# Optimization experiments

Hardware: AMD Instinct MI355X
Metric: run time of the kernel (lower is better)

The kernel has to match this reference:

```python
import jax, jax.numpy as jnp
import numpy as np
import math

DIM = 1280
NUM_HEADS = 16
HEAD_DIM = DIM // NUM_HEADS  # 80
MLP_HIDDEN = 4 * DIM         # 5120
N = 4096
EPS = 1e-6


def setup_inputs() -> dict:
    key = jax.random.key(0)
    ks = jax.random.split(key, 12)
    s = 0.02
    inp = {
        "hidden_states": jax.random.normal(ks[0], (N, DIM), jnp.float32),
        "rotary_pos_emb": jax.random.normal(ks[1], (N, HEAD_DIM // 2), jnp.float32),
        "cu_seqlens": jnp.array([0, 1024, 2048, 3072, 4096], jnp.int32),
        "norm1_w": jnp.ones((DIM,), jnp.float32),
        "norm1_b": jnp.zeros((DIM,), jnp.float32),
        "norm2_w": jnp.ones((DIM,), jnp.float32),
        "norm2_b": jnp.zeros((DIM,), jnp.float32),
        "qkv_w": jax.random.normal(ks[2], (3 * DIM, DIM), jnp.float32) * s,
        "qkv_b": jnp.zeros((3 * DIM,), jnp.float32),
        "proj_w": jax.random.normal(ks[3], (DIM, DIM), jnp.float32) * s,
        "proj_b": jnp.zeros((DIM,), jnp.float32),
        "fc1_w": jax.random.normal(ks[4], (MLP_HIDDEN, DIM), jnp.float32) * s,
        "fc1_b": jnp.zeros((MLP_HIDDEN,), jnp.float32),
        "fc2_w": jax.random.normal(ks[5], (DIM, MLP_HIDDEN), jnp.float32) * s,
        "fc2_b": jnp.zeros((DIM,), jnp.float32),
    }
    return inp


def _layernorm(x, w, b):
    m = jnp.mean(x, axis=-1, keepdims=True)
    v = jnp.mean(jnp.square(x - m), axis=-1, keepdims=True)
    return (x - m) * jax.lax.rsqrt(v + EPS) * w + b


def _apply_rope(t, cos, sin):
    # t: [N, H, hd]; cos/sin: [N, 1, hd]
    x1 = t[..., : HEAD_DIM // 2]
    x2 = t[..., HEAD_DIM // 2:]
    rot = jnp.concatenate([-x2, x1], axis=-1)
    return t * cos + rot * sin


def _quick_gelu(x):
    return x * jax.nn.sigmoid(1.702 * x)


def reference(hidden_states, rotary_pos_emb, cu_seqlens,
              norm1_w, norm1_b, norm2_w, norm2_b,
              qkv_w, qkv_b, proj_w, proj_b,
              fc1_w, fc1_b, fc2_w, fc2_b):
    n = hidden_states.shape[0]
    # ---- attention branch (pre-norm) ----
    x = _layernorm(hidden_states, norm1_w, norm1_b)
    qkv = (x @ qkv_w.T + qkv_b).reshape(n, 3, NUM_HEADS, HEAD_DIM)
    q, k, v = qkv[:, 0], qkv[:, 1], qkv[:, 2]  # [N, H, hd]
    # rotary: freqs [N, hd//2] -> tiled cos/sin [N, 1, hd]
    cos = jnp.cos(rotary_pos_emb)
    sin = jnp.sin(rotary_pos_emb)
    cos = jnp.concatenate([cos, cos], axis=-1)[:, None, :]
    sin = jnp.concatenate([sin, sin], axis=-1)[:, None, :]
    q = _apply_rope(q, cos, sin)
    k = _apply_rope(k, cos, sin)
    # block-diagonal varlen mask from cu_seqlens via segment ids
    seg = jnp.searchsorted(cu_seqlens[1:], jnp.arange(n, dtype=cu_seqlens.dtype), side="right")
    allowed = seg[:, None] == seg[None, :]  # [N, N] bool
    scores = jnp.einsum("qhd,khd->hqk", q, k) / math.sqrt(HEAD_DIM)
    scores = jnp.where(allowed[None], scores, jnp.finfo(scores.dtype).min)
    attn = jax.nn.softmax(scores.astype(jnp.float32), axis=-1).astype(q.dtype)
    out = jnp.einsum("hqk,khd->qhd", attn, v).reshape(n, DIM)
    out = out @ proj_w.T + proj_b
    h = hidden_states + out
    # ---- MLP branch (pre-norm) ----
    y = _layernorm(h, norm2_w, norm2_b)
    y = _quick_gelu(y @ fc1_w.T + fc1_b) @ fc2_w.T + fc2_b
    return h + y
```

## Files before the change

kernel.cpp:

```cpp
#include <hip/hip_runtime.h>
#include <hip/hip_bf16.h>


typedef __bf16 bf16_t;
typedef bf16_t bf16x8 __attribute__((ext_vector_type(8)));
typedef bf16_t bf16x4 __attribute__((ext_vector_type(4)));
typedef float f32x4 __attribute__((ext_vector_type(4)));

#define DIM 1280
#define NHEADS 16
#define HDIM 80
#define MLP 5120
#define NTOK 4096
#define QKV_N 3840

#define GLOAD_LDS16(gp, lp)                                                          \
    __builtin_amdgcn_global_load_lds((const __attribute__((address_space(1))) void*)(gp), \
                                     (__attribute__((address_space(3))) void*)(lp), 16, 0, 0)

__global__ void cvt_f32_bf16(const float* __restrict__ in, bf16_t* __restrict__ out, int n) {
    int i = (blockIdx.x * blockDim.x + threadIdx.x) * 4;
    int stride = gridDim.x * blockDim.x * 4;
    for (; i < n; i += stride) {
        float4 v = *(const float4*)(in + i);
        bf16x4 o;
        o[0] = (bf16_t)v.x; o[1] = (bf16_t)v.y; o[2] = (bf16_t)v.z; o[3] = (bf16_t)v.w;
        *(bf16x4*)(out + i) = o;
    }
}

__global__ void seg_kernel(const int* __restrict__ cu, int ncu, int* __restrict__ seg, int n) {
    int i = blockIdx.x * blockDim.x + threadIdx.x;
    if (i >= n) return;
    int s = 0;
    for (int j = 1; j < ncu - 1; j++) if (i >= cu[j]) s = j;
    seg[i] = s;
}

__global__ __launch_bounds__(256) void ln_kernel(const float* __restrict__ x,
                                                 const float* __restrict__ w,
                                                 const float* __restrict__ b,
                                                 bf16_t* __restrict__ out) {
    int row = blockIdx.x;
    const float* xr = x + (long)row * DIM;
    float v[5];
    float s = 0.f, ss = 0.f;
#pragma unroll
    for (int j = 0; j < 5; j++) {
        v[j] = xr[j * 256 + threadIdx.x];
        s += v[j];
        ss += v[j] * v[j];
    }
#pragma unroll
    for (int off = 32; off > 0; off >>= 1) {
        s += __shfl_xor(s, off, 64);
        ss += __shfl_xor(ss, off, 64);
    }
    __shared__ float red[8];
    int wid = threadIdx.x >> 6;
    if ((threadIdx.x & 63) == 0) { red[wid] = s; red[wid + 4] = ss; }
    __syncthreads();
    s = red[0] + red[1] + red[2] + red[3];
    ss = red[4] + red[5] + red[6] + red[7];
    float mean = s * (1.f / DIM);
    float var = ss * (1.f / DIM) - mean * mean;
    float rstd = rsqrtf(var + 1e-6f);
    bf16_t* orow = out + (long)row * DIM;
#pragma unroll
    for (int j = 0; j < 5; j++) {
        int d = j * 256 + threadIdx.x;
        orow[d] = (bf16_t)((v[j] - mean) * rstd * w[d] + b[d]);
    }
}

__global__ __launch_bounds__(256) void prep_kernel(const bf16_t* __restrict__ qkv,
                                                   const float* __restrict__ rot,
                                                   bf16_t* __restrict__ Qd,
                                                   bf16_t* __restrict__ Kd,
                                                   bf16_t* __restrict__ Vt) {
    __shared__ bf16_t tv[64 * 88];
    const int tid = threadIdx.x;
    const int t0 = blockIdx.x * 64;
    const int h = blockIdx.y;

    for (int c = tid; c < 64 * 10; c += 256) {
        int tl = c / 10, a = c % 10;
        bf16x8 v = *(const bf16x8*)(qkv + (long)(t0 + tl) * QKV_N + 2 * DIM + h * HDIM + a * 8);
        *(bf16x8*)(tv + tl * 88 + a * 8) = v;
    }

    for (int c = tid; c < 64 * 10; c += 256) {
        int tl = c / 10, a = c % 10;
        long gq = (long)(t0 + tl) * QKV_N + h * HDIM + a * 4;
        bf16x4 q1 = *(const bf16x4*)(qkv + gq);
        bf16x4 q2 = *(const bf16x4*)(qkv + gq + 40);
        bf16x4 k1 = *(const bf16x4*)(qkv + gq + DIM);
        bf16x4 k2 = *(const bf16x4*)(qkv + gq + DIM + 40);
        float4 rv = *(const float4*)(rot + (long)(t0 + tl) * 40 + a * 4);
        float rr[4] = {rv.x, rv.y, rv.z, rv.w};
        bf16x4 oq1, oq2, ok1, ok2;
#pragma unroll
        for (int j = 0; j < 4; j++) {
            float c_, s_;
            __sincosf(rr[j], &s_, &c_);
            float x1 = (float)q1[j], x2 = (float)q2[j];
            oq1[j] = (bf16_t)(x1 * c_ - x2 * s_);
            oq2[j] = (bf16_t)(x2 * c_ + x1 * s_);
            x1 = (float)k1[j]; x2 = (float)k2[j];
            ok1[j] = (bf16_t)(x1 * c_ - x2 * s_);
            ok2[j] = (bf16_t)(x2 * c_ + x1 * s_);
        }
        long o = ((long)h * NTOK + t0 + tl) * 96 + a * 4;
        *(bf16x4*)(Qd + o) = oq1;
        *(bf16x4*)(Qd + o + 40) = oq2;
        *(bf16x4*)(Kd + o) = ok1;
        *(bf16x4*)(Kd + o + 40) = ok2;
    }
    {
        bf16x8 z;
#pragma unroll
        for (int j = 0; j < 8; j++) z[j] = (bf16_t)0.f;
        for (int c = tid; c < 64 * 2; c += 256) {
            int tl = c / 2, a = c % 2;
            long o = ((long)h * NTOK + t0 + tl) * 96 + 80 + a * 8;
            *(bf16x8*)(Qd + o) = z;
            *(bf16x8*)(Kd + o) = z;
        }
    }
    __syncthreads();

    for (int c = tid; c < 80 * 8; c += 256) {
        int d = c / 8, tc = c % 8;
        bf16x8 v;
#pragma unroll
        for (int j = 0; j < 8; j++) v[j] = tv[(tc * 8 + j) * 88 + d];
        *(bf16x8*)(Vt + ((long)h * HDIM + d) * NTOK + t0 + tc * 8) = v;
    }
}

__global__ void fc2_reduce(const float* __restrict__ p, const float* __restrict__ b,
                           float* __restrict__ out) {
    long i = (long)blockIdx.x * blockDim.x + threadIdx.x;
    float4 o = ((const float4*)out)[i];
    float4 a0 = ((const float4*)p)[i];
    float4 a1 = ((const float4*)p)[i + (long)NTOK * DIM / 4];
    int c4 = (int)(i % (DIM / 4)) * 4;
    float4 bv = *(const float4*)(b + c4);
    o.x += a0.x + a1.x + bv.x;
    o.y += a0.y + a1.y + bv.y;
    o.z += a0.z + a1.z + bv.z;
    o.w += a0.w + a1.w + bv.w;
    ((float4*)out)[i] = o;
}

template <int EPI, int NF>
__global__ __launch_bounds__(512, 2) void gemm256(const bf16_t* __restrict__ A,
                                                  const bf16_t* __restrict__ B,
                                                  const float* __restrict__ bias,
                                                  const float* __restrict__ res,
                                                  void* __restrict__ Cv,
                                                  int M, int N, int K, int kspl) {
    constexpr int SLOTB = 32768 + NF * 8192;
    __shared__ char lds[2 * SLOTB];
    const int tid = threadIdx.x;
    const int lane = tid & 63;
    const int l15 = lane & 15;
    const int g = lane >> 4;
    const int wid = tid >> 6;
    const int wr = wid >> 2;
    const int wc = wid & 3;

    const int nx = gridDim.x;
    const int id = blockIdx.y * nx + blockIdx.x;
    const int cpx = (nx * gridDim.y) >> 3;
    const int sid = (id & 7) * cpx + (id >> 3);
    const int m0 = (sid / nx) * 256;
    const int n0 = (sid % nx) * (NF * 64);
    const int k0 = blockIdx.z * kspl;
    const int NT = kspl >> 6;

    const bf16_t* gA[4]; int lAo[4];
#pragma unroll
    for (int j = 0; j < 4; j++) {
        int off = j * 8192 + tid * 16;
        int row = off >> 7;
        int cb = (off & 127) ^ ((row & 7) << 4);
        gA[j] = A + (long)(m0 + row) * K + k0 + (cb >> 1);
        lAo[j] = j * 8192 + wid * 1024;
    }
    const bf16_t* gB[NF]; int lBo[NF];
#pragma unroll
    for (int j = 0; j < NF; j++) {
        int off = j * 8192 + tid * 16;
        int row = off >> 7;
        int cb = (off & 127) ^ ((row & 7) << 4);
        gB[j] = B + (long)(n0 + row) * K + k0 + (cb >> 1);
        lBo[j] = 32768 + j * 8192 + wid * 1024;
    }

    f32x4 acc[8][NF];
#pragma unroll
    for (int i = 0; i < 8; i++)
#pragma unroll
        for (int j = 0; j < NF; j++) acc[i][j] = (f32x4){0.f, 0.f, 0.f, 0.f};

    auto stage = [&](int slot, int t) {
        char* sb = lds + slot * SLOTB;
#pragma unroll
        for (int j = 0; j < 4; j++) GLOAD_LDS16(gA[j] + t * 64, sb + lAo[j]);
#pragma unroll
        for (int j = 0; j < NF; j++) GLOAD_LDS16(gB[j] + t * 64, sb + lBo[j]);
    };

    auto tile_body = [&](int slot) {
        const char* pA = lds + slot * SLOTB;
        const char* pB = pA + 32768;
#pragma unroll
        for (int ks = 0; ks < 2; ks++) {
            bf16x8 af[8], bb[NF];
#pragma unroll
            for (int n = 0; n < NF; n++) {
                int r = wc * (NF * 16) + n * 16 + l15;
                bb[n] = *(const bf16x8*)(pB + r * 128 + ((ks * 64 + g * 16) ^ ((r & 7) << 4)));
            }
#pragma unroll
            for (int m = 0; m < 8; m++) {
                int r = wr * 128 + m * 16 + l15;
                af[m] = *(const bf16x8*)(pA + r * 128 + ((ks * 64 + g * 16) ^ ((r & 7) << 4)));
            }
            asm volatile("s_waitcnt lgkmcnt(0)" ::: "memory");
            __builtin_amdgcn_sched_barrier(0);
            __builtin_amdgcn_s_setprio(1);
#pragma unroll
            for (int m = 0; m < 8; m++)
#pragma unroll
                for (int n = 0; n < NF; n++)
                    acc[m][n] = __builtin_amdgcn_mfma_f32_16x16x32_bf16(af[m], bb[n],
                                                                        acc[m][n], 0, 0, 0);
            __builtin_amdgcn_s_setprio(0);
        }
    };

    stage(0, 0);
    stage(1, 1);

    for (int t = 0; t < NT; ++t) {
        if (t < NT - 1) {
            if constexpr (NF == 4)
                asm volatile("s_waitcnt vmcnt(8)\n\ts_barrier" ::: "memory");
            else
                asm volatile("s_waitcnt vmcnt(9)\n\ts_barrier" ::: "memory");
        } else {
            asm volatile("s_waitcnt vmcnt(0)\n\ts_barrier" ::: "memory");
        }
        tile_body(t & 1);
        if (t + 2 < NT) {
            asm volatile("s_barrier" ::: "memory");
            stage(t & 1, t + 2);
        }
    }

#pragma unroll
    for (int m = 0; m < 8; m++)
#pragma unroll
        for (int n = 0; n < NF; n++) {
            const int col = n0 + wc * (NF * 16) + n * 16 + l15;
            const float bv = (EPI == 3) ? 0.f : bias[col];
#pragma unroll
            for (int rr = 0; rr < 4; rr++) {
                const int row = m0 + wr * 128 + m * 16 + g * 4 + rr;
                const long idx = (long)row * N + col;
                float val = acc[m][n][rr] + bv;
                if (EPI == 0) {
                    ((bf16_t*)Cv)[idx] = (bf16_t)val;
                } else if (EPI == 1) {
                    ((float*)Cv)[idx] = res[idx] + val;
                } else if (EPI == 2) {
                    float ge = val / (1.f + __expf(-1.702f * val));
                    ((bf16_t*)Cv)[idx] = (bf16_t)ge;
                } else {
                    ((float*)Cv)[(long)blockIdx.z * M * N + idx] = val;
                }
            }
        }
}

__global__ __launch_bounds__(256) void attn_kernel(const bf16_t* __restrict__ Qd,
                                                   const bf16_t* __restrict__ Kd,
                                                   const bf16_t* __restrict__ Vt,
                                                   const int* __restrict__ seg,
                                                   const int* __restrict__ cu,
                                                   bf16_t* __restrict__ out) {
    __shared__ bf16_t lK[64 * 104];
    __shared__ bf16_t lV[80 * 72];
    __shared__ bf16_t lP[4 * 16 * 72];

    const int tid = threadIdx.x;
    const int lane = tid & 63;
    const int l15 = lane & 15;
    const int g = lane >> 4;
    const int wid = tid >> 6;
    const int h = blockIdx.y;
    const int q0 = blockIdx.x * 64;

    bf16x8 aq[3];
    {
        const bf16_t* qp = Qd + ((long)h * NTOK + q0 + wid * 16 + l15) * 96;
#pragma unroll
        for (int ks = 0; ks < 3; ks++)
            aq[ks] = *(const bf16x8*)(qp + ks * 32 + g * 8);
    }
    int segq[4];
#pragma unroll
    for (int r = 0; r < 4; r++) segq[r] = seg[q0 + wid * 16 + g * 4 + r];
    const int kbeg = cu[seg[q0]];
    const int kend = cu[seg[q0 + 63] + 1];

    const float scale = 0.111803398874989485f;
    float mI[4], lI[4];
    f32x4 o[5];
#pragma unroll
    for (int r = 0; r < 4; r++) { mI[r] = -1e30f; lI[r] = 0.f; }
#pragma unroll
    for (int n = 0; n < 5; n++) o[n] = (f32x4){0.f, 0.f, 0.f, 0.f};

    for (int kt = kbeg; kt < kend; kt += 64) {
        for (int c = tid; c < 64 * 12; c += 256) {
            int row = c / 12, c16 = c % 12;
            bf16x8 v = *(const bf16x8*)(Kd + ((long)h * NTOK + kt + row) * 96 + c16 * 8);
            *(bf16x8*)(lK + row * 104 + c16 * 8) = v;
        }
        for (int c = tid; c < 80 * 8; c += 256) {
            int d = c / 8, a = c % 8;
            bf16x8 v = *(const bf16x8*)(Vt + ((long)h * HDIM + d) * NTOK + kt + a * 8);
            *(bf16x8*)(lV + d * 72 + a * 8) = v;
        }
        __syncthreads();

        f32x4 s[4];
#pragma unroll
        for (int n = 0; n < 4; n++) s[n] = (f32x4){0.f, 0.f, 0.f, 0.f};
#pragma unroll
        for (int n = 0; n < 4; n++)
#pragma unroll
            for (int ks = 0; ks < 3; ks++) {
                bf16x8 kf = *(const bf16x8*)(lK + (n * 16 + l15) * 104 + ks * 32 + g * 8);
                s[n] = __builtin_amdgcn_mfma_f32_16x16x32_bf16(aq[ks], kf, s[n], 0, 0, 0);
            }

        float sv[4][4];
#pragma unroll
        for (int n = 0; n < 4; n++) {
            int kg = kt + n * 16 + l15;
            int sk = seg[kg];
#pragma unroll
            for (int r = 0; r < 4; r++)
                sv[n][r] = (sk == segq[r]) ? s[n][r] * scale : -3.0e38f;
        }

        float nm[4], al[4], ps[4];
#pragma unroll
        for (int r = 0; r < 4; r++) {
            float x = fmaxf(fmaxf(sv[0][r], sv[1][r]), fmaxf(sv[2][r], sv[3][r]));
#pragma unroll
            for (int off = 8; off >= 1; off >>= 1) x = fmaxf(x, __shfl_xor(x, off, 64));
            nm[r] = fmaxf(mI[r], x);
            al[r] = __expf(mI[r] - nm[r]);
            ps[r] = 0.f;
        }
#pragma unroll
        for (int n = 0; n < 4; n++)
#pragma unroll
            for (int r = 0; r < 4; r++) {
                float p = __expf(sv[n][r] - nm[r]);
                ps[r] += p;
                lP[wid * 1152 + (g * 4 + r) * 72 + n * 16 + l15] = (bf16_t)p;
            }
#pragma unroll
        for (int r = 0; r < 4; r++) {
            float x = ps[r];
#pragma unroll
            for (int off = 8; off >= 1; off >>= 1) x += __shfl_xor(x, off, 64);
            lI[r] = lI[r] * al[r] + x;
            mI[r] = nm[r];
        }
#pragma unroll
        for (int n = 0; n < 5; n++)
#pragma unroll
            for (int r = 0; r < 4; r++) o[n][r] *= al[r];

        asm volatile("s_waitcnt lgkmcnt(0)" ::: "memory");
        bf16x8 pa[2];
#pragma unroll
        for (int ks = 0; ks < 2; ks++)
            pa[ks] = *(const bf16x8*)(lP + wid * 1152 + l15 * 72 + ks * 32 + g * 8);
#pragma unroll
        for (int n = 0; n < 5; n++)
#pragma unroll
            for (int ks = 0; ks < 2; ks++) {
                bf16x8 vb = *(const bf16x8*)(lV + (n * 16 + l15) * 72 + ks * 32 + g * 8);
                o[n] = __builtin_amdgcn_mfma_f32_16x16x32_bf16(pa[ks], vb, o[n], 0, 0, 0);
            }
        __syncthreads();
    }

#pragma unroll
    for (int n = 0; n < 5; n++)
#pragma unroll
        for (int r = 0; r < 4; r++) {
            int row = q0 + wid * 16 + g * 4 + r;
            out[(long)row * DIM + h * HDIM + n * 16 + l15] = (bf16_t)(o[n][r] / lI[r]);
        }
}

extern "C" void kernel_launch(void* const* d_in, const int* in_sizes, int n_in,
                              void* d_out, int out_size, void* d_ws, size_t ws_size,
                              hipStream_t stream) {
    const float* hidden = (const float*)d_in[0];
    const float* rot    = (const float*)d_in[1];
    const int*   cu     = (const int*)d_in[2];
    const float* n1w    = (const float*)d_in[3];
    const float* n1b    = (const float*)d_in[4];
    const float* n2w    = (const float*)d_in[5];
    const float* n2b    = (const float*)d_in[6];
    const float* qkv_w  = (const float*)d_in[7];
    const float* qkv_b  = (const float*)d_in[8];
    const float* proj_w = (const float*)d_in[9];
    const float* proj_b = (const float*)d_in[10];
    const float* fc1_w  = (const float*)d_in[11];
    const float* fc1_b  = (const float*)d_in[12];
    const float* fc2_w  = (const float*)d_in[13];
    const float* fc2_b  = (const float*)d_in[14];
    float* outp = (float*)d_out;

    char* ws = (char*)d_ws;
    bf16_t* w2   = (bf16_t*)(ws);
    bf16_t* w1   = (bf16_t*)(ws + 13107200);
    bf16_t* wp   = (bf16_t*)(ws + 26214400);
    bf16_t* wq   = (bf16_t*)(ws + 29491200);
    bf16_t* xln  = (bf16_t*)(ws + 39321600);
    bf16_t* qkvb = (bf16_t*)(ws + 49807360);
    bf16_t* Qd   = (bf16_t*)(ws + 81264640);
    bf16_t* Kd   = (bf16_t*)(ws + 93847552);
    bf16_t* Vt   = (bf16_t*)(ws + 106430464);
    bf16_t* attno= (bf16_t*)(ws + 116916224);
    bf16_t* act  = (bf16_t*)(ws + 49807360);
    float*  p01  = (float*)(ws + 91750400);
    int*    seg  = (int*)(ws + 133693440);

    int ncu = in_sizes[2];

    cvt_f32_bf16<<<2048, 256, 0, stream>>>(qkv_w, wq, QKV_N * DIM);
    cvt_f32_bf16<<<1024, 256, 0, stream>>>(proj_w, wp, DIM * DIM);
    cvt_f32_bf16<<<2048, 256, 0, stream>>>(fc1_w, w1, MLP * DIM);
    cvt_f32_bf16<<<2048, 256, 0, stream>>>(fc2_w, w2, DIM * MLP);
    seg_kernel<<<(NTOK + 255) / 256, 256, 0, stream>>>(cu, ncu, seg, NTOK);

    ln_kernel<<<NTOK, 256, 0, stream>>>(hidden, n1w, n1b, xln);
    gemm256<0, 5><<<dim3(QKV_N / 320, NTOK / 256, 1), 512, 0, stream>>>(
        xln, wq, qkv_b, nullptr, qkvb, NTOK, QKV_N, DIM, DIM);
    prep_kernel<<<dim3(NTOK / 64, NHEADS), 256, 0, stream>>>(qkvb, rot, Qd, Kd, Vt);
    attn_kernel<<<dim3(NTOK / 64, NHEADS), 256, 0, stream>>>(Qd, Kd, Vt, seg, cu, attno);
    gemm256<1, 4><<<dim3(DIM / 256, NTOK / 256, 1), 512, 0, stream>>>(
        attno, wp, proj_b, hidden, outp, NTOK, DIM, DIM, DIM);
    ln_kernel<<<NTOK, 256, 0, stream>>>(outp, n2w, n2b, xln);
    gemm256<2, 5><<<dim3(MLP / 320, NTOK / 256, 1), 512, 0, stream>>>(
        xln, w1, fc1_b, nullptr, act, NTOK, MLP, DIM, DIM);
    gemm256<3, 4><<<dim3(DIM / 256, NTOK / 256, 2), 512, 0, stream>>>(
        act, w2, nullptr, nullptr, p01, NTOK, DIM, MLP, 2560);
    fc2_reduce<<<NTOK * DIM / 4 / 256, 256, 0, stream>>>(p01, fc2_b, outp);
}
```

Measured before the change: 378.8 us.

## Rewrite GEMM with 4-stage BK=32 LDS pipeline and split-K proj

Replaces the double-buffered BK=64 GEMM, which had variable N-tile width, with a fixed 256x256-tile kernel. The new kernel uses BK=32 slices in four LDS buffers, prefetching three tiles ahead and issuing the next stage before the MMA work to overlap loads with compute. The proj GEMM becomes a split-K=2 GEMM writing fp32 partials, followed by a reduce kernel that adds bias and the residual, so the small 80-block grid gets more parallelism. The cost is extra partial-sum memory traffic and an additional launch, plus a different QKV/FC1 tile shape with more blocks.

```diff
diff --git a/kernel.cpp b/kernel.cpp
--- a/kernel.cpp
+++ b/kernel.cpp
@@ -138,30 +138,27 @@
     }
 }
 
-__global__ void fc2_reduce(const float* __restrict__ p, const float* __restrict__ b,
-                           float* __restrict__ out) {
+__global__ void reduce2(const float* __restrict__ p, const float* __restrict__ b,
+                        const float* __restrict__ res, float* __restrict__ out) {
     long i = (long)blockIdx.x * blockDim.x + threadIdx.x;
-    float4 o = ((const float4*)out)[i];
+    float4 r = ((const float4*)res)[i];
     float4 a0 = ((const float4*)p)[i];
     float4 a1 = ((const float4*)p)[i + (long)NTOK * DIM / 4];
     int c4 = (int)(i % (DIM / 4)) * 4;
     float4 bv = *(const float4*)(b + c4);
-    o.x += a0.x + a1.x + bv.x;
-    o.y += a0.y + a1.y + bv.y;
-    o.z += a0.z + a1.z + bv.z;
-    o.w += a0.w + a1.w + bv.w;
+    float4 o = {r.x + a0.x + a1.x + bv.x, r.y + a0.y + a1.y + bv.y,
+                r.z + a0.z + a1.z + bv.z, r.w + a0.w + a1.w + bv.w};
     ((float4*)out)[i] = o;
 }
 
-template <int EPI, int NF>
-__global__ __launch_bounds__(512, 2) void gemm256(const bf16_t* __restrict__ A,
-                                                  const bf16_t* __restrict__ B,
-                                                  const float* __restrict__ bias,
-                                                  const float* __restrict__ res,
-                                                  void* __restrict__ Cv,
-                                                  int M, int N, int K, int kspl) {
-    constexpr int SLOTB = 32768 + NF * 8192;
-    __shared__ char lds[2 * SLOTB];
+template <int EPI>
+__global__ __launch_bounds__(512, 2) void gemmP(const bf16_t* __restrict__ A,
+                                                const bf16_t* __restrict__ B,
+                                                const float* __restrict__ bias,
+                                                const float* __restrict__ res,
+                                                void* __restrict__ Cv,
+                                                int M, int N, int K, int kspl) {
+    __shared__ char lds[4 * 32768];
     const int tid = threadIdx.x;
     const int lane = tid & 63;
     const int l15 = lane & 15;
@@ -175,96 +172,77 @@
     const int cpx = (nx * gridDim.y) >> 3;
     const int sid = (id & 7) * cpx + (id >> 3);
     const int m0 = (sid / nx) * 256;
-    const int n0 = (sid % nx) * (NF * 64);
+    const int n0 = (sid % nx) * 256;
     const int k0 = blockIdx.z * kspl;
-    const int NT = kspl >> 6;
-
-    const bf16_t* gA[4]; int lAo[4];
-#pragma unroll
-    for (int j = 0; j < 4; j++) {
+    const int NT = kspl >> 5;
+
+    const bf16_t* gA[2]; const bf16_t* gB[2]; int lAo[2], lBo[2];
+#pragma unroll
+    for (int j = 0; j < 2; j++) {
         int off = j * 8192 + tid * 16;
-        int row = off >> 7;
-        int cb = (off & 127) ^ ((row & 7) << 4);
+        int row = off >> 6;
+        int cb = (off & 63) ^ ((row & 3) << 4);
         gA[j] = A + (long)(m0 + row) * K + k0 + (cb >> 1);
+        gB[j] = B + (long)(n0 + row) * K + k0 + (cb >> 1);
         lAo[j] = j * 8192 + wid * 1024;
-    }
-    const bf16_t* gB[NF]; int lBo[NF];
-#pragma unroll
-    for (int j = 0; j < NF; j++) {
-        int off = j * 8192 + tid * 16;
-        int row = off >> 7;
-        int cb = (off & 127) ^ ((row & 7) << 4);
-        gB[j] = B + (long)(n0 + row) * K + k0 + (cb >> 1);
-        lBo[j] = 32768 + j * 8192 + wid * 1024;
-    }
-
-    f32x4 acc[8][NF];
+        lBo[j] = 16384 + j * 8192 + wid * 1024;
+    }
+
+    f32x4 acc[8][4];
 #pragma unroll
     for (int i = 0; i < 8; i++)
 #pragma unroll
-        for (int j = 0; j < NF; j++) acc[i][j] = (f32x4){0.f, 0.f, 0.f, 0.f};
-
-    auto stage = [&](int slot, int t) {
-        char* sb = lds + slot * SLOTB;
-#pragma unroll
-        for (int j = 0; j < 4; j++) GLOAD_LDS16(gA[j] + t * 64, sb + lAo[j]);
-#pragma unroll
-        for (int j = 0; j < NF; j++) GLOAD_LDS16(gB[j] + t * 64, sb + lBo[j]);
-    };
-
-    auto tile_body = [&](int slot) {
-        const char* pA = lds + slot * SLOTB;
-        const char* pB = pA + 32768;
-#pragma unroll
-        for (int ks = 0; ks < 2; ks++) {
-            bf16x8 af[8], bb[NF];
-#pragma unroll
-            for (int n = 0; n < NF; n++) {
-                int r = wc * (NF * 16) + n * 16 + l15;
-                bb[n] = *(const bf16x8*)(pB + r * 128 + ((ks * 64 + g * 16) ^ ((r & 7) << 4)));
-            }
-#pragma unroll
-            for (int m = 0; m < 8; m++) {
-                int r = wr * 128 + m * 16 + l15;
-                af[m] = *(const bf16x8*)(pA + r * 128 + ((ks * 64 + g * 16) ^ ((r & 7) << 4)));
-            }
-            asm volatile("s_waitcnt lgkmcnt(0)" ::: "memory");
-            __builtin_amdgcn_sched_barrier(0);
-            __builtin_amdgcn_s_setprio(1);
-#pragma unroll
-            for (int m = 0; m < 8; m++)
-#pragma unroll
-                for (int n = 0; n < NF; n++)
-                    acc[m][n] = __builtin_amdgcn_mfma_f32_16x16x32_bf16(af[m], bb[n],
-                                                                        acc[m][n], 0, 0, 0);
-            __builtin_amdgcn_s_setprio(0);
-        }
+        for (int j = 0; j < 4; j++) acc[i][j] = (f32x4){0.f, 0.f, 0.f, 0.f};
+
+    auto stage = [&](int buf, int t) {
+        char* sb = lds + buf * 32768;
+#pragma unroll
+        for (int j = 0; j < 2; j++) GLOAD_LDS16(gA[j] + t * 32, sb + lAo[j]);
+#pragma unroll
+        for (int j = 0; j < 2; j++) GLOAD_LDS16(gB[j] + t * 32, sb + lBo[j]);
     };
 
     stage(0, 0);
     stage(1, 1);
+    stage(2, 2);
 
     for (int t = 0; t < NT; ++t) {
-        if (t < NT - 1) {
-            if constexpr (NF == 4)
-                asm volatile("s_waitcnt vmcnt(8)\n\ts_barrier" ::: "memory");
-            else
-                asm volatile("s_waitcnt vmcnt(9)\n\ts_barrier" ::: "memory");
-        } else {
-            asm volatile("s_waitcnt vmcnt(0)\n\ts_barrier" ::: "memory");
-        }
-        tile_body(t & 1);
-        if (t + 2 < NT) {
-            asm volatile("s_barrier" ::: "memory");
-            stage(t & 1, t + 2);
-        }
+        if (t < NT - 2)
+            asm volatile("s_waitcnt vmcnt(8) lgkmcnt(0)\n\ts_barrier" ::: "memory");
+        else if (t == NT - 2)
+            asm volatile("s_waitcnt vmcnt(4) lgkmcnt(0)\n\ts_barrier" ::: "memory");
+        else
+            asm volatile("s_waitcnt vmcnt(0) lgkmcnt(0)\n\ts_barrier" ::: "memory");
+        if (t + 3 < NT) stage((t + 3) & 3, t + 3);
+
+        const char* pA = lds + (t & 3) * 32768;
+        const char* pB = pA + 16384;
+        bf16x8 af[8], bb[4];
+#pragma unroll
+        for (int n = 0; n < 4; n++) {
+            int r = wc * 64 + n * 16 + l15;
+            bb[n] = *(const bf16x8*)(pB + r * 64 + ((g * 16) ^ ((r & 3) << 4)));
+        }
+#pragma unroll
+        for (int m = 0; m < 8; m++) {
+            int r = wr * 128 + m * 16 + l15;
+            af[m] = *(const bf16x8*)(pA + r * 64 + ((g * 16) ^ ((r & 3) << 4)));
+        }
+        __builtin_amdgcn_s_setprio(1);
+#pragma unroll
+        for (int m = 0; m < 8; m++)
+#pragma unroll
+            for (int n = 0; n < 4; n++)
+                acc[m][n] = __builtin_amdgcn_mfma_f32_16x16x32_bf16(af[m], bb[n],
+                                                                    acc[m][n], 0, 0, 0);
+        __builtin_amdgcn_s_setprio(0);
     }
 
 #pragma unroll
     for (int m = 0; m < 8; m++)
 #pragma unroll
-        for (int n = 0; n < NF; n++) {
-            const int col = n0 + wc * (NF * 16) + n * 16 + l15;
+        for (int n = 0; n < 4; n++) {
+            const int col = n0 + wc * 64 + n * 16 + l15;
             const float bv = (EPI == 3) ? 0.f : bias[col];
 #pragma unroll
             for (int rr = 0; rr < 4; rr++) {
@@ -440,6 +418,7 @@
     bf16_t* wq   = (bf16_t*)(ws + 29491200);
     bf16_t* xln  = (bf16_t*)(ws + 39321600);
     bf16_t* qkvb = (bf16_t*)(ws + 49807360);
+    float*  projp= (float*)(ws + 49807360);
     bf16_t* Qd   = (bf16_t*)(ws + 81264640);
     bf16_t* Kd   = (bf16_t*)(ws + 93847552);
     bf16_t* Vt   = (bf16_t*)(ws + 106430464);
@@ -457,16 +436,17 @@
     seg_kernel<<<(NTOK + 255) / 256, 256, 0, stream>>>(cu, ncu, seg, NTOK);
 
     ln_kernel<<<NTOK, 256, 0, stream>>>(hidden, n1w, n1b, xln);
-    gemm256<0, 5><<<dim3(QKV_N / 320, NTOK / 256, 1), 512, 0, stream>>>(
+    gemmP<0><<<dim3(QKV_N / 256, NTOK / 256, 1), 512, 0, stream>>>(
         xln, wq, qkv_b, nullptr, qkvb, NTOK, QKV_N, DIM, DIM);
     prep_kernel<<<dim3(NTOK / 64, NHEADS), 256, 0, stream>>>(qkvb, rot, Qd, Kd, Vt);
     attn_kernel<<<dim3(NTOK / 64, NHEADS), 256, 0, stream>>>(Qd, Kd, Vt, seg, cu, attno);
-    gemm256<1, 4><<<dim3(DIM / 256, NTOK / 256, 1), 512, 0, stream>>>(
-        attno, wp, proj_b, hidden, outp, NTOK, DIM, DIM, DIM);
+    gemmP<3><<<dim3(DIM / 256, NTOK / 256, 2), 512, 0, stream>>>(
+        attno, wp, nullptr, nullptr, projp, NTOK, DIM, DIM, 640);
+    reduce2<<<NTOK * DIM / 4 / 256, 256, 0, stream>>>(projp, proj_b, hidden, outp);
     ln_kernel<<<NTOK, 256, 0, stream>>>(outp, n2w, n2b, xln);
-    gemm256<2, 5><<<dim3(MLP / 320, NTOK / 256, 1), 512, 0, stream>>>(
+    gemmP<2><<<dim3(MLP / 256, NTOK / 256, 1), 512, 0, stream>>>(
         xln, w1, fc1_b, nullptr, act, NTOK, MLP, DIM, DIM);
-    gemm256<3, 4><<<dim3(DIM / 256, NTOK / 256, 2), 512, 0, stream>>>(
+    gemmP<3><<<dim3(DIM / 256, NTOK / 256, 2), 512, 0, stream>>>(
         act, w2, nullptr, nullptr, p01, NTOK, DIM, MLP, 2560);
-    fc2_reduce<<<NTOK * DIM / 4 / 256, 256, 0, stream>>>(p01, fc2_b, outp);
-}
+    reduce2<<<NTOK * DIM / 4 / 256, 256, 0, stream>>>(p01, fc2_b, outp, outp);
+}
```

Result: slower. 409.0 us (+8.0%).
